# Optimization experiments

Measured on AMD Instinct MI355X. Metric: run time of the kernel, lower is better.

## Reference

```python
import jax, jax.numpy as jnp
import numpy as np

B, NQ, NK, H, DV = 4, 128, 1024, 256, 256
NEG_INF = -1e6


def setup_inputs() -> dict:
    key = jax.random.key(0)
    ks = jax.random.split(key, 7)
    return {
        "queries": jax.random.normal(ks[0], (B, NQ, H), dtype=jnp.float32),
        "keys": jax.random.normal(ks[1], (B, NK, H), dtype=jnp.float32),
        "values": jax.random.normal(ks[2], (B, NK, DV), dtype=jnp.float32),
        "valid_lens": jax.random.randint(ks[3], (B,), 1, NK + 1, dtype=jnp.int32),
        "Wq": jax.random.normal(ks[4], (H, H), dtype=jnp.float32) * (1.0 / np.sqrt(H)),
        "Wk": jax.random.normal(ks[5], (H, H), dtype=jnp.float32) * (1.0 / np.sqrt(H)),
        "wv": jax.random.normal(ks[6], (H,), dtype=jnp.float32) * (1.0 / np.sqrt(H)),
    }


def reference(queries, keys, values, valid_lens, Wq, Wk, wv):
    # Project queries and keys: nn.Linear(x) = x @ W.T
    q = jnp.einsum('bqd,hd->bqh', queries, Wq)  # (B,NQ,H)
    k = jnp.einsum('bkd,hd->bkh', keys, Wk)     # (B,NK,H)
    # Broadcasted add -> tanh -> scalar projection: (B,NQ,NK,H) intermediate
    features = jnp.tanh(q[:, :, None, :] + k[:, None, :, :])
    scores = jnp.einsum('bqkh,h->bqk', features, wv)  # (B,NQ,NK)
    # masked_softmax over the key axis: positions >= valid_len get -1e6
    mask = jnp.arange(scores.shape[-1])[None, None, :] < valid_lens[:, None, None]
    scores = jnp.where(mask, scores, NEG_INF)
    attn = jax.nn.softmax(scores, axis=-1)  # (B,NQ,NK)
    # dropout p=0.0 (identity). Weighted sum over values.
    return jnp.einsum('bqk,bkv->bqv', attn, values)  # (B,NQ,DV)
```

## Files before the change

### kernel.cpp

```cpp
#include <hip/hip_runtime.h>
#include <hip/hip_bf16.h>
#include <cmath>

#define B 4
#define NQ 128
#define NK 1024
#define HD 256
#define DV 256

__global__ __launch_bounds__(256) void proj_tanh(const float* __restrict__ X,
                                                 const float* __restrict__ W,
                                                 const float* __restrict__ wv,
                                                 float* __restrict__ wt_out,
                                                 float* __restrict__ t_out)
{
    __shared__ float sX[64][68];
    __shared__ float sW[64][68];
    const int tid = threadIdx.x;
    const int bm = blockIdx.x * 64;
    const int bh = blockIdx.y * 64;
    const int ty = tid >> 4, tx = tid & 15;
    const int lr = tid >> 2;
    const int lc = (tid & 3) << 4;

    float acc[4][4] = {};

    for (int ks = 0; ks < HD; ks += 64) {
        #pragma unroll
        for (int j = 0; j < 4; ++j) {
            const int d = lc + j * 4;
            float4 xv = *(const float4*)&X[(size_t)(bm + lr) * HD + ks + d];
            float4 wm = *(const float4*)&W[(size_t)(bh + lr) * HD + ks + d];
            sX[d + 0][lr] = xv.x; sX[d + 1][lr] = xv.y;
            sX[d + 2][lr] = xv.z; sX[d + 3][lr] = xv.w;
            sW[d + 0][lr] = wm.x; sW[d + 1][lr] = wm.y;
            sW[d + 2][lr] = wm.z; sW[d + 3][lr] = wm.w;
        }
        __syncthreads();
        #pragma unroll 8
        for (int kk = 0; kk < 64; ++kk) {
            float4 a4 = *(const float4*)&sX[kk][ty * 4];
            float4 b4 = *(const float4*)&sW[kk][tx * 4];
            float av[4] = {a4.x, a4.y, a4.z, a4.w};
            float bv[4] = {b4.x, b4.y, b4.z, b4.w};
            #pragma unroll
            for (int i = 0; i < 4; ++i)
                #pragma unroll
                for (int j = 0; j < 4; ++j)
                    acc[i][j] = fmaf(av[i], bv[j], acc[i][j]);
        }
        __syncthreads();
    }

    const int m0 = bm + ty * 4;
    const int h0 = bh + tx * 4;
    float4 wv4 = *(const float4*)&wv[h0];
    float wvv[4] = {wv4.x, wv4.y, wv4.z, wv4.w};
    #pragma unroll
    for (int i = 0; i < 4; ++i) {
        float t[4];
        #pragma unroll
        for (int j = 0; j < 4; ++j) t[j] = tanhf(acc[i][j]);
        float4 t4  = {t[0], t[1], t[2], t[3]};
        float4 wt4 = {wvv[0] * t[0], wvv[1] * t[1], wvv[2] * t[2], wvv[3] * t[3]};
        *(float4*)&t_out[(size_t)(m0 + i) * HD + h0]  = t4;
        *(float4*)&wt_out[(size_t)(m0 + i) * HD + h0] = wt4;
    }
}

__global__ __launch_bounds__(256) void scores_kernel(const float* __restrict__ wtq,
                                                     const float* __restrict__ tq,
                                                     const float* __restrict__ wtk,
                                                     const float* __restrict__ tk,
                                                     float* __restrict__ scores)
{
    __shared__ float s_qw[32][68];
    __shared__ float s_qt[32][68];
    __shared__ float s_kw[32][68];
    __shared__ float s_kt[32][68];
    const int tid = threadIdx.x;
    const int kb = blockIdx.x * 32;
    const int qb = blockIdx.y * 32;
    const int b  = blockIdx.z;
    const int ty = tid >> 4, tx = tid & 15;

    float acc00 = 0.f, acc01 = 0.f, acc10 = 0.f, acc11 = 0.f;
    const size_t qbase = ((size_t)b * NQ + qb) * HD;
    const size_t kbase = ((size_t)b * NK + kb) * HD;

    for (int hc = 0; hc < HD; hc += 64) {
        #pragma unroll
        for (int f0 = 0; f0 < 2; ++f0) {
            const int f   = tid + f0 * 256;
            const int row = f >> 4;
            const int col = (f & 15) << 2;
            const int prow = (row >> 1) | ((row & 1) << 4);
            *(float4*)&s_qw[row][col]  = *(const float4*)&wtq[qbase + (size_t)row * HD + hc + col];
            *(float4*)&s_qt[row][col]  = *(const float4*)&tq [qbase + (size_t)row * HD + hc + col];
            *(float4*)&s_kw[prow][col] = *(const float4*)&wtk[kbase + (size_t)row * HD + hc + col];
            *(float4*)&s_kt[prow][col] = *(const float4*)&tk [kbase + (size_t)row * HD + hc + col];
        }
        __syncthreads();

        const int q0 = ty * 2, q1 = q0 + 1;
        const int k0 = tx, k1 = tx + 16;

        #pragma unroll
        for (int i = 0; i < 16; ++i) {
            const int h4 = i << 2;
            float4 v;
            v = *(const float4*)&s_qw[q0][h4]; float qw0[4] = {v.x, v.y, v.z, v.w};
            v = *(const float4*)&s_qt[q0][h4]; float qt0[4] = {v.x, v.y, v.z, v.w};
            v = *(const float4*)&s_qw[q1][h4]; float qw1[4] = {v.x, v.y, v.z, v.w};
            v = *(const float4*)&s_qt[q1][h4]; float qt1[4] = {v.x, v.y, v.z, v.w};
            v = *(const float4*)&s_kw[k0][h4]; float kw0[4] = {v.x, v.y, v.z, v.w};
            v = *(const float4*)&s_kt[k0][h4]; float kt0[4] = {v.x, v.y, v.z, v.w};
            v = *(const float4*)&s_kw[k1][h4]; float kw1[4] = {v.x, v.y, v.z, v.w};
            v = *(const float4*)&s_kt[k1][h4]; float kt1[4] = {v.x, v.y, v.z, v.w};
            #pragma unroll
            for (int j = 0; j < 4; ++j) {
                float n, d;
                n = qw0[j] + kw0[j]; d = fmaf(qt0[j], kt0[j], 1.0f);
                acc00 = fmaf(n, __builtin_amdgcn_rcpf(d), acc00);
                n = qw0[j] + kw1[j]; d = fmaf(qt0[j], kt1[j], 1.0f);
                acc01 = fmaf(n, __builtin_amdgcn_rcpf(d), acc01);
                n = qw1[j] + kw0[j]; d = fmaf(qt1[j], kt0[j], 1.0f);
                acc10 = fmaf(n, __builtin_amdgcn_rcpf(d), acc10);
                n = qw1[j] + kw1[j]; d = fmaf(qt1[j], kt1[j], 1.0f);
                acc11 = fmaf(n, __builtin_amdgcn_rcpf(d), acc11);
            }
        }
        __syncthreads();
    }

    const int qg = qb + ty * 2;
    const int kg = kb + tx * 2;
    const size_t sbase = ((size_t)b * NQ + qg) * NK + kg;
    *(float2*)&scores[sbase]      = make_float2(acc00, acc01);
    *(float2*)&scores[sbase + NK] = make_float2(acc10, acc11);
}

__global__ __launch_bounds__(256) void softmax_kernel(float* __restrict__ scores,
                                                      const int* __restrict__ valid_lens)
{
    const int row = blockIdx.x;
    const int b = row >> 7;
    const int valid = valid_lens[b];
    float* s = scores + (size_t)row * NK;
    const int tid = threadIdx.x;

    float4 v = *(const float4*)&s[tid * 4];
    float x[4] = {v.x, v.y, v.z, v.w};
    #pragma unroll
    for (int j = 0; j < 4; ++j) {
        const int k = tid * 4 + j;
        if (k >= valid) x[j] = -1e6f;
    }
    float m = fmaxf(fmaxf(x[0], x[1]), fmaxf(x[2], x[3]));
    #pragma unroll
    for (int off = 32; off >= 1; off >>= 1)
        m = fmaxf(m, __shfl_xor(m, off));

    __shared__ float redm[4], reds[4];
    const int wid = tid >> 6, lane = tid & 63;
    if (lane == 0) redm[wid] = m;
    __syncthreads();
    m = fmaxf(fmaxf(redm[0], redm[1]), fmaxf(redm[2], redm[3]));

    float p[4], psum = 0.f;
    #pragma unroll
    for (int j = 0; j < 4; ++j) { p[j] = __expf(x[j] - m); psum += p[j]; }
    #pragma unroll
    for (int off = 32; off >= 1; off >>= 1)
        psum += __shfl_xor(psum, off);
    if (lane == 0) reds[wid] = psum;
    __syncthreads();
    const float total = reds[0] + reds[1] + reds[2] + reds[3];
    const float inv = 1.0f / total;

    float4 o = {p[0] * inv, p[1] * inv, p[2] * inv, p[3] * inv};
    *(float4*)&s[tid * 4] = o;
}

__global__ __launch_bounds__(256) void pv_partial(const float* __restrict__ attn,
                                                  const float* __restrict__ values,
                                                  float* __restrict__ partial)
{
    __shared__ float s_a[16][128];
    const int tid = threadIdx.x;
    const int ks = blockIdx.x, qg = blockIdx.y, b = blockIdx.z;
    const int q0 = qg * 16;
    const int k0 = ks * 128;

    #pragma unroll
    for (int f0 = 0; f0 < 2; ++f0) {
        const int f = tid + f0 * 256;
        const int row = f >> 5;
        const int col = (f & 31) << 2;
        *(float4*)&s_a[row][col] =
            *(const float4*)&attn[((size_t)b * NQ + q0 + row) * NK + k0 + col];
    }
    __syncthreads();

    float acc[16] = {};
    #pragma unroll 8
    for (int k = 0; k < 128; ++k) {
        const float va = values[((size_t)b * NK + k0 + k) * DV + tid];
        #pragma unroll
        for (int q = 0; q < 16; ++q)
            acc[q] = fmaf(s_a[q][k], va, acc[q]);
    }

    const size_t pbase = (size_t)ks * (B * NQ * DV) + ((size_t)b * NQ + q0) * DV + tid;
    #pragma unroll
    for (int q = 0; q < 16; ++q)
        partial[pbase + (size_t)q * DV] = acc[q];
}

__global__ __launch_bounds__(256) void reduce_pv(const float* __restrict__ partial,
                                                 float* __restrict__ out)
{
    const int i = blockIdx.x * 256 + threadIdx.x;
    float s = 0.f;
    #pragma unroll
    for (int p = 0; p < 8; ++p) s += partial[(size_t)p * (B * NQ * DV) + i];
    out[i] = s;
}

extern "C" void kernel_launch(void* const* d_in, const int* in_sizes, int n_in,
                              void* d_out, int out_size, void* d_ws, size_t ws_size,
                              hipStream_t stream) {
    const float* queries   = (const float*)d_in[0];
    const float* keys      = (const float*)d_in[1];
    const float* values    = (const float*)d_in[2];
    const int*   valid_lens= (const int*)  d_in[3];
    const float* Wq        = (const float*)d_in[4];
    const float* Wk        = (const float*)d_in[5];
    const float* wv        = (const float*)d_in[6];
    float* out = (float*)d_out;

    float* ws      = (float*)d_ws;
    float* wtq     = ws;
    float* tq      = wtq + (size_t)B * NQ * HD;
    float* wtk     = tq  + (size_t)B * NQ * HD;
    float* tk      = wtk + (size_t)B * NK * HD;
    float* scores  = tk  + (size_t)B * NK * HD;
    float* partial = scores + (size_t)B * NQ * NK;

    proj_tanh<<<dim3((B * NQ) / 64, HD / 64), 256, 0, stream>>>(queries, Wq, wv, wtq, tq);
    proj_tanh<<<dim3((B * NK) / 64, HD / 64), 256, 0, stream>>>(keys, Wk, wv, wtk, tk);
    scores_kernel<<<dim3(NK / 32, NQ / 32, B), 256, 0, stream>>>(wtq, tq, wtk, tk, scores);
    softmax_kernel<<<dim3(B * NQ), 256, 0, stream>>>(scores, valid_lens);
    pv_partial<<<dim3(8, NQ / 16, B), 256, 0, stream>>>(scores, values, partial);
    reduce_pv<<<dim3((B * NQ * DV) / 256), 256, 0, stream>>>(partial, out);
}
```

Before: 152.2 us.

## Rewrite tanh-sum scoring via exp form and batch four reciprocals per quad

The projections now store exp(2x) instead of tanh and its weighted copy. Using tanh(a+b) = 1 - 2/(1+e^{2a}e^{2b}), the score becomes a weighted sum of 1/(1+EqEk) plus a per-row constant that softmax cancels. Four terms are combined over a common denominator so only one reciprocal is needed per four h values. The two projection launches are merged into one grid, and the scores kernel now reads two shared tiles instead of four. The exp(2x) values can overflow for large projections, and the product of four denominators could overflow to inf, which risks NaN or accuracy loss.

```diff
diff --git a/kernel.cpp b/kernel.cpp
--- a/kernel.cpp
+++ b/kernel.cpp
@@ -8,12 +8,17 @@
 #define HD 256
 #define DV 256
 
-__global__ __launch_bounds__(256) void proj_tanh(const float* __restrict__ X,
-                                                 const float* __restrict__ W,
-                                                 const float* __restrict__ wv,
-                                                 float* __restrict__ wt_out,
-                                                 float* __restrict__ t_out)
-{
+__global__ __launch_bounds__(256) void proj_exp(
+    const float* __restrict__ Xq, const float* __restrict__ Xk,
+    const float* __restrict__ Wq, const float* __restrict__ Wk,
+    float* __restrict__ Eq, float* __restrict__ Ek)
+{
+    const int z = blockIdx.z;
+    if (z == 0 && blockIdx.x >= (B * NQ) / 64) return;
+    const float* __restrict__ X = z ? Xk : Xq;
+    const float* __restrict__ W = z ? Wk : Wq;
+    float* __restrict__ E = z ? Ek : Eq;
+
     __shared__ float sX[64][68];
     __shared__ float sW[64][68];
     const int tid = threadIdx.x;
@@ -54,90 +59,92 @@
 
     const int m0 = bm + ty * 4;
     const int h0 = bh + tx * 4;
-    float4 wv4 = *(const float4*)&wv[h0];
-    float wvv[4] = {wv4.x, wv4.y, wv4.z, wv4.w};
     #pragma unroll
     for (int i = 0; i < 4; ++i) {
-        float t[4];
-        #pragma unroll
-        for (int j = 0; j < 4; ++j) t[j] = tanhf(acc[i][j]);
-        float4 t4  = {t[0], t[1], t[2], t[3]};
-        float4 wt4 = {wvv[0] * t[0], wvv[1] * t[1], wvv[2] * t[2], wvv[3] * t[3]};
-        *(float4*)&t_out[(size_t)(m0 + i) * HD + h0]  = t4;
-        *(float4*)&wt_out[(size_t)(m0 + i) * HD + h0] = wt4;
-    }
-}
-
-__global__ __launch_bounds__(256) void scores_kernel(const float* __restrict__ wtq,
-                                                     const float* __restrict__ tq,
-                                                     const float* __restrict__ wtk,
-                                                     const float* __restrict__ tk,
-                                                     float* __restrict__ scores)
-{
-    __shared__ float s_qw[32][68];
-    __shared__ float s_qt[32][68];
-    __shared__ float s_kw[32][68];
-    __shared__ float s_kt[32][68];
+        float4 e4 = {__expf(2.0f * acc[i][0]), __expf(2.0f * acc[i][1]),
+                     __expf(2.0f * acc[i][2]), __expf(2.0f * acc[i][3])};
+        *(float4*)&E[(size_t)(m0 + i) * HD + h0] = e4;
+    }
+}
+
+__device__ __forceinline__ void quad_acc(float& acc, float4 q, float4 k, float4 w)
+{
+    float d0 = fmaf(q.x, k.x, 1.0f);
+    float d1 = fmaf(q.y, k.y, 1.0f);
+    float d2 = fmaf(q.z, k.z, 1.0f);
+    float d3 = fmaf(q.w, k.w, 1.0f);
+    float n01 = fmaf(w.x, d1, w.y * d0);
+    float d01 = d0 * d1;
+    float n23 = fmaf(w.z, d3, w.w * d2);
+    float d23 = d2 * d3;
+    float n  = fmaf(n01, d23, n23 * d01);
+    float dd = d01 * d23;
+    acc = fmaf(n, __builtin_amdgcn_rcpf(dd), acc);
+}
+
+__global__ __launch_bounds__(256) void scores_kernel(
+    const float* __restrict__ Eq, const float* __restrict__ Ek,
+    const float* __restrict__ wv, float* __restrict__ scores)
+{
+    __shared__ float s_q[32][68];
+    __shared__ float s_k[32][68];
+    __shared__ float s_w[64];
     const int tid = threadIdx.x;
     const int kb = blockIdx.x * 32;
     const int qb = blockIdx.y * 32;
     const int b  = blockIdx.z;
     const int ty = tid >> 4, tx = tid & 15;
 
-    float acc00 = 0.f, acc01 = 0.f, acc10 = 0.f, acc11 = 0.f;
+    float a00 = 0.f, a01 = 0.f, a10 = 0.f, a11 = 0.f;
     const size_t qbase = ((size_t)b * NQ + qb) * HD;
     const size_t kbase = ((size_t)b * NK + kb) * HD;
 
+    const int srow = tid >> 3;
+    const int scol = (tid & 7) << 3;
+
     for (int hc = 0; hc < HD; hc += 64) {
-        #pragma unroll
-        for (int f0 = 0; f0 < 2; ++f0) {
-            const int f   = tid + f0 * 256;
-            const int row = f >> 4;
-            const int col = (f & 15) << 2;
-            const int prow = (row >> 1) | ((row & 1) << 4);
-            *(float4*)&s_qw[row][col]  = *(const float4*)&wtq[qbase + (size_t)row * HD + hc + col];
-            *(float4*)&s_qt[row][col]  = *(const float4*)&tq [qbase + (size_t)row * HD + hc + col];
-            *(float4*)&s_kw[prow][col] = *(const float4*)&wtk[kbase + (size_t)row * HD + hc + col];
-            *(float4*)&s_kt[prow][col] = *(const float4*)&tk [kbase + (size_t)row * HD + hc + col];
-        }
-        __syncthreads();
-
-        const int q0 = ty * 2, q1 = q0 + 1;
-        const int k0 = tx, k1 = tx + 16;
-
+        {
+            const float* qp = &Eq[qbase + (size_t)srow * HD + hc + scol];
+            const float* kp = &Ek[kbase + (size_t)srow * HD + hc + scol];
+            float4 q0 = *(const float4*)qp;
+            float4 q1 = *(const float4*)(qp + 4);
+            float4 k0 = *(const float4*)kp;
+            float4 k1 = *(const float4*)(kp + 4);
+            *(float4*)&s_q[srow][scol]     = q0;
+            *(float4*)&s_q[srow][scol + 4] = q1;
+            *(float4*)&s_k[srow][scol]     = k0;
+            *(float4*)&s_k[srow][scol + 4] = k1;
+            if (tid < 16) {
+                float4 w = *(const float4*)&wv[hc + tid * 4];
+                s_w[tid * 4 + 0] = -2.0f * w.x;
+                s_w[tid * 4 + 1] = -2.0f * w.y;
+                s_w[tid * 4 + 2] = -2.0f * w.z;
+                s_w[tid * 4 + 3] = -2.0f * w.w;
+            }
+        }
+        __syncthreads();
         #pragma unroll
         for (int i = 0; i < 16; ++i) {
             const int h4 = i << 2;
-            float4 v;
-            v = *(const float4*)&s_qw[q0][h4]; float qw0[4] = {v.x, v.y, v.z, v.w};
-            v = *(const float4*)&s_qt[q0][h4]; float qt0[4] = {v.x, v.y, v.z, v.w};
-            v = *(const float4*)&s_qw[q1][h4]; float qw1[4] = {v.x, v.y, v.z, v.w};
-            v = *(const float4*)&s_qt[q1][h4]; float qt1[4] = {v.x, v.y, v.z, v.w};
-            v = *(const float4*)&s_kw[k0][h4]; float kw0[4] = {v.x, v.y, v.z, v.w};
-            v = *(const float4*)&s_kt[k0][h4]; float kt0[4] = {v.x, v.y, v.z, v.w};
-            v = *(const float4*)&s_kw[k1][h4]; float kw1[4] = {v.x, v.y, v.z, v.w};
-            v = *(const float4*)&s_kt[k1][h4]; float kt1[4] = {v.x, v.y, v.z, v.w};
-            #pragma unroll
-            for (int j = 0; j < 4; ++j) {
-                float n, d;
-                n = qw0[j] + kw0[j]; d = fmaf(qt0[j], kt0[j], 1.0f);
-                acc00 = fmaf(n, __builtin_amdgcn_rcpf(d), acc00);
-                n = qw0[j] + kw1[j]; d = fmaf(qt0[j], kt1[j], 1.0f);
-                acc01 = fmaf(n, __builtin_amdgcn_rcpf(d), acc01);
-                n = qw1[j] + kw0[j]; d = fmaf(qt1[j], kt0[j], 1.0f);
-                acc10 = fmaf(n, __builtin_amdgcn_rcpf(d), acc10);
-                n = qw1[j] + kw1[j]; d = fmaf(qt1[j], kt1[j], 1.0f);
-                acc11 = fmaf(n, __builtin_amdgcn_rcpf(d), acc11);
-            }
-        }
-        __syncthreads();
-    }
-
-    const int qg = qb + ty * 2;
-    const int kg = kb + tx * 2;
-    const size_t sbase = ((size_t)b * NQ + qg) * NK + kg;
-    *(float2*)&scores[sbase]      = make_float2(acc00, acc01);
-    *(float2*)&scores[sbase + NK] = make_float2(acc10, acc11);
+            const float4 W4 = *(const float4*)&s_w[h4];
+            const float4 Q0 = *(const float4*)&s_q[ty][h4];
+            const float4 Q1 = *(const float4*)&s_q[ty + 16][h4];
+            const float4 K0 = *(const float4*)&s_k[tx][h4];
+            const float4 K1 = *(const float4*)&s_k[tx + 16][h4];
+            quad_acc(a00, Q0, K0, W4);
+            quad_acc(a01, Q0, K1, W4);
+            quad_acc(a10, Q1, K0, W4);
+            quad_acc(a11, Q1, K1, W4);
+        }
+        __syncthreads();
+    }
+
+    const size_t r0 = ((size_t)b * NQ + qb + ty) * NK;
+    const size_t r1 = ((size_t)b * NQ + qb + ty + 16) * NK;
+    scores[r0 + kb + tx]      = a00;
+    scores[r0 + kb + tx + 16] = a01;
+    scores[r1 + kb + tx]      = a10;
+    scores[r1 + kb + tx + 16] = a11;
 }
 
 __global__ __launch_bounds__(256) void softmax_kernel(float* __restrict__ scores,
@@ -230,26 +237,24 @@
 extern "C" void kernel_launch(void* const* d_in, const int* in_sizes, int n_in,
                               void* d_out, int out_size, void* d_ws, size_t ws_size,
                               hipStream_t stream) {
-    const float* queries   = (const float*)d_in[0];
-    const float* keys      = (const float*)d_in[1];
-    const float* values    = (const float*)d_in[2];
-    const int*   valid_lens= (const int*)  d_in[3];
-    const float* Wq        = (const float*)d_in[4];
-    const float* Wk        = (const float*)d_in[5];
-    const float* wv        = (const float*)d_in[6];
+    const float* queries    = (const float*)d_in[0];
+    const float* keys       = (const float*)d_in[1];
+    const float* values     = (const float*)d_in[2];
+    const int*   valid_lens = (const int*)  d_in[3];
+    const float* Wq         = (const float*)d_in[4];
+    const float* Wk         = (const float*)d_in[5];
+    const float* wv         = (const float*)d_in[6];
     float* out = (float*)d_out;
 
     float* ws      = (float*)d_ws;
-    float* wtq     = ws;
-    float* tq      = wtq + (size_t)B * NQ * HD;
-    float* wtk     = tq  + (size_t)B * NQ * HD;
-    float* tk      = wtk + (size_t)B * NK * HD;
-    float* scores  = tk  + (size_t)B * NK * HD;
+    float* Eq      = ws;
+    float* Ek      = Eq + (size_t)B * NQ * HD;
+    float* scores  = Ek + (size_t)B * NK * HD;
     float* partial = scores + (size_t)B * NQ * NK;
 
-    proj_tanh<<<dim3((B * NQ) / 64, HD / 64), 256, 0, stream>>>(queries, Wq, wv, wtq, tq);
-    proj_tanh<<<dim3((B * NK) / 64, HD / 64), 256, 0, stream>>>(keys, Wk, wv, wtk, tk);
-    scores_kernel<<<dim3(NK / 32, NQ / 32, B), 256, 0, stream>>>(wtq, tq, wtk, tk, scores);
+    proj_exp<<<dim3((B * NK) / 64, HD / 64, 2), 256, 0, stream>>>(
+        queries, keys, Wq, Wk, Eq, Ek);
+    scores_kernel<<<dim3(NK / 32, NQ / 32, B), 256, 0, stream>>>(Eq, Ek, wv, scores);
     softmax_kernel<<<dim3(B * NQ), 256, 0, stream>>>(scores, valid_lens);
     pv_partial<<<dim3(8, NQ / 16, B), 256, 0, stream>>>(scores, values, partial);
     reduce_pv<<<dim3((B * NQ * DV) / 256), 256, 0, stream>>>(partial, out);
```

Result: faster. 129.1 us (-15.1%).
